# Performance work log

Measured on AMD Instinct MI355X. Metric: run time of the kernel, lower is better.

## Reference

```python
import jax, jax.numpy as jnp
import numpy as np

B, T, F, H, A, D = 1024, 256, 128, 128, 8, 256


def setup_inputs() -> dict:
    key = jax.random.key(0)
    ks = jax.random.split(key, 16)
    s = lambda k, shape, scale: jax.random.normal(k, shape, dtype=jnp.float32) * scale
    return {
        "h": jax.random.normal(ks[0], (B, T, F), dtype=jnp.float32),
        # LSTM params (flax LSTMCell: input kernel no bias, hidden kernel with bias; gate order i,f,g,o)
        "Wx": s(ks[1], (F, 4 * H), 1.0 / np.sqrt(F)),
        "Wh": s(ks[2], (H, 4 * H), 1.0 / np.sqrt(H)),
        "bh": jnp.zeros((4 * H,), jnp.float32),
        # actor head
        "Wa1": s(ks[3], (H, D), np.sqrt(2.0 / H)),
        "ba1": jnp.zeros((D,), jnp.float32),
        "Wa2": s(ks[4], (D, D), np.sqrt(2.0 / D)),
        "ba2": jnp.zeros((D,), jnp.float32),
        "Wa3": s(ks[5], (D, A), 0.01 / np.sqrt(D)),
        "ba3": jnp.zeros((A,), jnp.float32),
        "log_std": jnp.zeros((A,), jnp.float32),
        # critic head
        "Wc1": s(ks[6], (H, D), np.sqrt(2.0 / H)),
        "bc1": jnp.zeros((D,), jnp.float32),
        "Wc2": s(ks[7], (D, D), np.sqrt(2.0 / D)),
        "bc2": jnp.zeros((D,), jnp.float32),
        "Wc3": s(ks[8], (D, 1), 1.0 / np.sqrt(D)),
        "bc3": jnp.zeros((1,), jnp.float32),
    }


def reference(h, Wx, Wh, bh, Wa1, ba1, Wa2, ba2, Wa3, ba3, log_std,
              Wc1, bc1, Wc2, bc2, Wc3, bc3):
    act = jnp.tanh  # activation='tanh'
    # Precompute input projections for all gates: [B,T,4H] -> scan over time.
    xg = jnp.einsum('btf,fg->btg', h, Wx)
    c0 = jnp.zeros((h.shape[0], H), h.dtype)
    h0 = jnp.zeros((h.shape[0], H), h.dtype)

    def step(carry, xg_t):
        c, hs = carry
        z = xg_t + hs @ Wh + bh  # [B,4H]
        i = jax.nn.sigmoid(z[:, :H])
        f = jax.nn.sigmoid(z[:, H:2 * H])
        g = jnp.tanh(z[:, 2 * H:3 * H])
        o = jax.nn.sigmoid(z[:, 3 * H:])
        c = f * c + i * g
        hs = o * jnp.tanh(c)
        return (c, hs), None

    (_, x), _ = jax.lax.scan(step, (c0, h0), jnp.swapaxes(xg, 0, 1))  # x = last hidden [B,H]

    a = act(x @ Wa1 + ba1)
    a = act(a @ Wa2 + ba2)
    mean = a @ Wa3 + ba3                      # [B,A] policy mean
    std = jnp.exp(log_std)                    # [A] policy std (diag)

    v = act(x @ Wc1 + bc1)
    v = act(v @ Wc2 + bc2)
    value = (v @ Wc3 + bc3)                   # [B,1]

    # Pack (mean, std, value) as in (pi, critic): [B, 2A+1]
    return jnp.concatenate([mean, jnp.broadcast_to(std, mean.shape), value], axis=-1)
```

## Files before the change

### kernel.cpp

```cpp
#include <hip/hip_runtime.h>


typedef _Float16 f16x8 __attribute__((ext_vector_type(8)));
typedef _Float16 f16x4 __attribute__((ext_vector_type(4)));
typedef float    f32x4 __attribute__((ext_vector_type(4)));

#define NLOG2E (-1.4426950408889634f)

__device__ __forceinline__ float rcpf(float x) { return __builtin_amdgcn_rcpf(x); }
__device__ __forceinline__ float ex2(float x)  { return __builtin_amdgcn_exp2f(x); }

__device__ __forceinline__ f16x4 pack4(const float4 a) {
    f16x4 v;
    v[0] = (_Float16)a.x; v[1] = (_Float16)a.y;
    v[2] = (_Float16)a.z; v[3] = (_Float16)a.w;
    return v;
}

__global__ __launch_bounds__(512, 2)
void ac_fused(const float* __restrict__ hin,
              const float* __restrict__ Wx, const float* __restrict__ Wh,
              const float* __restrict__ bh,
              const float* __restrict__ Wa1, const float* __restrict__ ba1,
              const float* __restrict__ Wa2, const float* __restrict__ ba2,
              const float* __restrict__ Wa3, const float* __restrict__ ba3,
              const float* __restrict__ logstd,
              const float* __restrict__ Wc1, const float* __restrict__ bc1,
              const float* __restrict__ Wc2, const float* __restrict__ bc2,
              const float* __restrict__ Wc3, const float* __restrict__ bc3,
              float* __restrict__ out)
{
    constexpr int T = 256, F = 128, H = 128, G = 512;

    __shared__ f16x8 Abuf[2][256];
    __shared__ f16x8 Axg[2][256];
    __shared__ float xf[4][F + 1];
    __shared__ float hb[2][4][257];

    const int tid  = threadIdx.x;
    const int lane = tid & 63;
    const int wv   = tid >> 6;
    const int m16  = lane & 15;
    const int q    = lane >> 4;
    const int r0   = blockIdx.x << 2;
    const int ncol = (wv << 4) + m16;

    f16x8 bwx[4][4], bwh[4][4];
    #pragma unroll
    for (int kt = 0; kt < 4; ++kt) {
        #pragma unroll
        for (int s = 0; s < 4; ++s) {
            f16x8 vx, vh;
            #pragma unroll
            for (int j = 0; j < 8; ++j) {
                const int k = (kt << 5) + (q << 3) + j;
                vx[j] = (_Float16)Wx[k * G + s * H + ncol];
                vh[j] = (_Float16)Wh[k * G + s * H + ncol];
            }
            bwx[s][kt] = vx;
            bwh[s][kt] = vh;
        }
    }
    const float nbi = NLOG2E * bh[0 * H + ncol];
    const float nbf = NLOG2E * bh[1 * H + ncol];
    const float nbg = 2.0f * NLOG2E * bh[2 * H + ncol];
    const float nbo = NLOG2E * bh[3 * H + ncol];

    const int xc = tid >> 1;
    const int xh = tid & 1;
    const int xk0 = ((xc >> 6) << 5) + (((xc >> 4) & 3) << 3) + (xh << 2);
    const float* pgbase = hin + (size_t)(r0 + ((xc >> 2) & 3)) * T * F
                              + (size_t)(xc & 3) * F + xk0;

    const int hw0 = ((((ncol >> 5) << 6) + (((ncol >> 3) & 3) << 4) + (q << 2)) << 3)
                    + (ncol & 7);

    {
        f16x8 zz = {};
        ((f16x8*)Abuf)[tid] = zz;
    }

    {
        const float4 xp0 = *(const float4*)(pgbase);
        const float4 xp1 = *(const float4*)(pgbase + 4 * (size_t)F);
        __syncthreads();
        *(f16x4*)((_Float16*)&Axg[0][0] + xc * 8 + xh * 4) = pack4(xp0);
        *(f16x4*)((_Float16*)&Axg[1][0] + xc * 8 + xh * 4) = pack4(xp1);
    }
    asm volatile("s_waitcnt lgkmcnt(0)" ::: "memory");
    __builtin_amdgcn_s_barrier();

    float cstate = 0.0f;
    float hcur   = 0.0f;

    for (int t0 = 0; t0 < T; t0 += 8) {
        f32x4 P[2][4];
        #pragma unroll
        for (int mt = 0; mt < 2; ++mt)
            #pragma unroll
            for (int s = 0; s < 4; ++s) P[mt][s] = f32x4{0.f, 0.f, 0.f, 0.f};
        #pragma unroll
        for (int kt = 0; kt < 4; ++kt) {
            const f16x8 fr0 = Axg[0][(kt << 6) + lane];
            const f16x8 fr1 = Axg[1][(kt << 6) + lane];
            P[0][0] = __builtin_amdgcn_mfma_f32_16x16x32_f16(fr0, bwx[0][kt], P[0][0], 0, 0, 0);
            P[0][1] = __builtin_amdgcn_mfma_f32_16x16x32_f16(fr0, bwx[1][kt], P[0][1], 0, 0, 0);
            P[0][2] = __builtin_amdgcn_mfma_f32_16x16x32_f16(fr0, bwx[2][kt], P[0][2], 0, 0, 0);
            P[0][3] = __builtin_amdgcn_mfma_f32_16x16x32_f16(fr0, bwx[3][kt], P[0][3], 0, 0, 0);
            P[1][0] = __builtin_amdgcn_mfma_f32_16x16x32_f16(fr1, bwx[0][kt], P[1][0], 0, 0, 0);
            P[1][1] = __builtin_amdgcn_mfma_f32_16x16x32_f16(fr1, bwx[1][kt], P[1][1], 0, 0, 0);
            P[1][2] = __builtin_amdgcn_mfma_f32_16x16x32_f16(fr1, bwx[2][kt], P[1][2], 0, 0, 0);
            P[1][3] = __builtin_amdgcn_mfma_f32_16x16x32_f16(fr1, bwx[3][kt], P[1][3], 0, 0, 0);
        }

        float4 xp0n, xp1n;
        #pragma unroll
        for (int i = 0; i < 8; ++i) {
            const f16x8* Ac = &Abuf[i & 1][0];
            f16x8*       An = &Abuf[(i + 1) & 1][0];

            if (i == 2) {
                const int t0n = (t0 + 8 < T) ? t0 + 8 : t0;
                xp0n = *(const float4*)(pgbase + (size_t)t0n * F);
                xp1n = *(const float4*)(pgbase + (size_t)(t0n + 4) * F);
            }

            const f16x8 af0 = Ac[lane];
            const f16x8 af1 = Ac[64 + lane];
            const f16x8 af2 = Ac[128 + lane];
            const f16x8 af3 = Ac[192 + lane];

            const int mt = i >> 2, rg = i & 3;
            const float x0 = P[mt][0][rg], x1 = P[mt][1][rg];
            const float x2 = P[mt][2][rg], x3 = P[mt][3][rg];
            f32x4 a0 = {x0, x0, x0, x0}, a1 = {x1, x1, x1, x1};
            f32x4 a2 = {x2, x2, x2, x2}, a3 = {x3, x3, x3, x3};

            a0 = __builtin_amdgcn_mfma_f32_16x16x32_f16(af0, bwh[0][0], a0, 0, 0, 0);
            a1 = __builtin_amdgcn_mfma_f32_16x16x32_f16(af0, bwh[1][0], a1, 0, 0, 0);
            a2 = __builtin_amdgcn_mfma_f32_16x16x32_f16(af0, bwh[2][0], a2, 0, 0, 0);
            a3 = __builtin_amdgcn_mfma_f32_16x16x32_f16(af0, bwh[3][0], a3, 0, 0, 0);
            a0 = __builtin_amdgcn_mfma_f32_16x16x32_f16(af1, bwh[0][1], a0, 0, 0, 0);
            a1 = __builtin_amdgcn_mfma_f32_16x16x32_f16(af1, bwh[1][1], a1, 0, 0, 0);
            a2 = __builtin_amdgcn_mfma_f32_16x16x32_f16(af1, bwh[2][1], a2, 0, 0, 0);
            a3 = __builtin_amdgcn_mfma_f32_16x16x32_f16(af1, bwh[3][1], a3, 0, 0, 0);
            a0 = __builtin_amdgcn_mfma_f32_16x16x32_f16(af2, bwh[0][2], a0, 0, 0, 0);
            a1 = __builtin_amdgcn_mfma_f32_16x16x32_f16(af2, bwh[1][2], a1, 0, 0, 0);
            a2 = __builtin_amdgcn_mfma_f32_16x16x32_f16(af2, bwh[2][2], a2, 0, 0, 0);
            a3 = __builtin_amdgcn_mfma_f32_16x16x32_f16(af2, bwh[3][2], a3, 0, 0, 0);
            a0 = __builtin_amdgcn_mfma_f32_16x16x32_f16(af3, bwh[0][3], a0, 0, 0, 0);
            a1 = __builtin_amdgcn_mfma_f32_16x16x32_f16(af3, bwh[1][3], a1, 0, 0, 0);
            a2 = __builtin_amdgcn_mfma_f32_16x16x32_f16(af3, bwh[2][3], a2, 0, 0, 0);
            a3 = __builtin_amdgcn_mfma_f32_16x16x32_f16(af3, bwh[3][3], a3, 0, 0, 0);

            const float iv = rcpf(1.0f + ex2(fmaf(a0[0], NLOG2E, nbi)));
            const float fv = rcpf(1.0f + ex2(fmaf(a1[0], NLOG2E, nbf)));
            const float gv = 2.0f * rcpf(1.0f + ex2(fmaf(a2[0], 2.0f * NLOG2E, nbg))) - 1.0f;
            const float ov = rcpf(1.0f + ex2(fmaf(a3[0], NLOG2E, nbo)));
            cstate = fv * cstate + iv * gv;
            const float th = 2.0f * rcpf(1.0f + ex2(cstate * (2.0f * NLOG2E))) - 1.0f;
            hcur = ov * th;

            {
                const _Float16 hh = (_Float16)hcur;
                _Float16* hp = (_Float16*)An + hw0;
                hp[0]  = hh;
                hp[8]  = hh;
                hp[16] = hh;
                hp[24] = hh;
            }

            if (i == 7) {
                *(f16x4*)((_Float16*)&Axg[0][0] + xc * 8 + xh * 4) = pack4(xp0n);
                *(f16x4*)((_Float16*)&Axg[1][0] + xc * 8 + xh * 4) = pack4(xp1n);
            }

            asm volatile("s_waitcnt lgkmcnt(0)" ::: "memory");
            __builtin_amdgcn_s_barrier();
        }
    }

    xf[q][ncol] = hcur;
    __syncthreads();

    const int n  = tid & 255;
    const int rh = tid >> 8;

    auto tanhl = [&](float x) { return 2.0f * rcpf(1.0f + ex2(x * (2.0f * NLOG2E))) - 1.0f; };

    auto layer = [&](const float* __restrict__ W, const float* __restrict__ bv,
                     const float* xin, int xs, int K, float* yout, int ys) {
        float acc0, acc1;
        const float b = bv[n];
        acc0 = b; acc1 = b;
        #pragma unroll 4
        for (int k = 0; k < K; ++k) {
            const float w = W[k * 256 + n];
            acc0 += xin[(rh * 2 + 0) * xs + k] * w;
            acc1 += xin[(rh * 2 + 1) * xs + k] * w;
        }
        yout[(rh * 2 + 0) * ys + n] = tanhl(acc0);
        yout[(rh * 2 + 1) * ys + n] = tanhl(acc1);
    };

    layer(Wa1, ba1, &xf[0][0], F + 1, 128, &hb[0][0][0], 257);
    __syncthreads();
    layer(Wa2, ba2, &hb[0][0][0], 257, 256, &hb[1][0][0], 257);
    __syncthreads();
    layer(Wc1, bc1, &xf[0][0], F + 1, 128, &hb[0][0][0], 257);
    if (tid < 32) {
        const int r = tid >> 3, aa = tid & 7;
        float acc = ba3[aa];
        #pragma unroll 4
        for (int k = 0; k < 256; ++k) acc += hb[1][r][k] * Wa3[k * 8 + aa];
        out[(size_t)(r0 + r) * 17 + aa]     = acc;
        out[(size_t)(r0 + r) * 17 + 8 + aa] = __expf(logstd[aa]);
    }
    __syncthreads();
    layer(Wc2, bc2, &hb[0][0][0], 257, 256, &hb[1][0][0], 257);
    __syncthreads();
    if (tid < 4) {
        const int r = tid;
        float acc = bc3[0];
        #pragma unroll 4
        for (int k = 0; k < 256; ++k) acc += hb[1][r][k] * Wc3[k];
        out[(size_t)(r0 + r) * 17 + 16] = acc;
    }
}

extern "C" void kernel_launch(void* const* d_in, const int* in_sizes, int n_in,
                              void* d_out, int out_size, void* d_ws, size_t ws_size,
                              hipStream_t stream) {
    (void)in_sizes; (void)n_in; (void)d_ws; (void)ws_size; (void)out_size;
    const float* hin = (const float*)d_in[0];
    const float* Wx  = (const float*)d_in[1];
    const float* Wh  = (const float*)d_in[2];
    const float* bh  = (const float*)d_in[3];
    const float* Wa1 = (const float*)d_in[4];
    const float* ba1 = (const float*)d_in[5];
    const float* Wa2 = (const float*)d_in[6];
    const float* ba2 = (const float*)d_in[7];
    const float* Wa3 = (const float*)d_in[8];
    const float* ba3 = (const float*)d_in[9];
    const float* ls  = (const float*)d_in[10];
    const float* Wc1 = (const float*)d_in[11];
    const float* bc1 = (const float*)d_in[12];
    const float* Wc2 = (const float*)d_in[13];
    const float* bc2 = (const float*)d_in[14];
    const float* Wc3 = (const float*)d_in[15];
    const float* bc3 = (const float*)d_in[16];

    hipLaunchKernelGGL(ac_fused, dim3(256), dim3(512), 0, stream,
                       hin, Wx, Wh, bh, Wa1, ba1, Wa2, ba2, Wa3, ba3, ls,
                       Wc1, bc1, Wc2, bc2, Wc3, bc3, (float*)d_out);
}
```

Baseline: 425.6 us.

## Shrink hidden-state buffer, write h once, parallelize head reductions

The hidden-state LDS buffer is compacted from a replicated 256-entry A-fragment layout into a 16x4 layout. Each thread now writes its h value once instead of four times, and the MFMA A fragments are read with replicated row indices, which cuts LDS store traffic on the serial recurrent path. The final actor and critic projections are split across many threads with a partial-sum reduction in shared memory, in place of 32 or 4 threads running 256-long serial loops, and the MLP loop unroll factor is raised. The extra barriers and reduction buffers add a little overhead to the tail.

```diff
diff --git a/kernel.cpp b/kernel.cpp
--- a/kernel.cpp
+++ b/kernel.cpp
@@ -32,10 +32,12 @@
 {
     constexpr int T = 256, F = 128, H = 128, G = 512;
 
-    __shared__ f16x8 Abuf[2][256];
+    __shared__ f16x8 Hbuf[2][16][4];
     __shared__ f16x8 Axg[2][256];
     __shared__ float xf[4][F + 1];
     __shared__ float hb[2][4][257];
+    __shared__ float redA[4][8][8];
+    __shared__ float redC[4][32];
 
     const int tid  = threadIdx.x;
     const int lane = tid & 63;
@@ -72,12 +74,12 @@
     const float* pgbase = hin + (size_t)(r0 + ((xc >> 2) & 3)) * T * F
                               + (size_t)(xc & 3) * F + xk0;
 
-    const int hw0 = ((((ncol >> 5) << 6) + (((ncol >> 3) & 3) << 4) + (q << 2)) << 3)
-                    + (ncol & 7);
-
-    {
+    const int hr0 = (q << 2) + (m16 >> 2);
+    const int hw  = ((((ncol >> 3) << 2) + q) << 3) + (ncol & 7);
+
+    if (tid < 128) {
         f16x8 zz = {};
-        ((f16x8*)Abuf)[tid] = zz;
+        ((f16x8*)Hbuf)[tid] = zz;
     }
 
     {
@@ -116,8 +118,9 @@
         float4 xp0n, xp1n;
         #pragma unroll
         for (int i = 0; i < 8; ++i) {
-            const f16x8* Ac = &Abuf[i & 1][0];
-            f16x8*       An = &Abuf[(i + 1) & 1][0];
+            const int t = t0 + i;
+            const f16x8* Hc = &Hbuf[t & 1][0][0];
+            _Float16*    Hn = (_Float16*)&Hbuf[(t + 1) & 1][0][0];
 
             if (i == 2) {
                 const int t0n = (t0 + 8 < T) ? t0 + 8 : t0;
@@ -125,10 +128,10 @@
                 xp1n = *(const float4*)(pgbase + (size_t)(t0n + 4) * F);
             }
 
-            const f16x8 af0 = Ac[lane];
-            const f16x8 af1 = Ac[64 + lane];
-            const f16x8 af2 = Ac[128 + lane];
-            const f16x8 af3 = Ac[192 + lane];
+            const f16x8 af0 = Hc[hr0];
+            const f16x8 af1 = Hc[16 + hr0];
+            const f16x8 af2 = Hc[32 + hr0];
+            const f16x8 af3 = Hc[48 + hr0];
 
             const int mt = i >> 2, rg = i & 3;
             const float x0 = P[mt][0][rg], x1 = P[mt][1][rg];
@@ -161,14 +164,7 @@
             const float th = 2.0f * rcpf(1.0f + ex2(cstate * (2.0f * NLOG2E))) - 1.0f;
             hcur = ov * th;
 
-            {
-                const _Float16 hh = (_Float16)hcur;
-                _Float16* hp = (_Float16*)An + hw0;
-                hp[0]  = hh;
-                hp[8]  = hh;
-                hp[16] = hh;
-                hp[24] = hh;
-            }
+            Hn[hw] = (_Float16)hcur;
 
             if (i == 7) {
                 *(f16x4*)((_Float16*)&Axg[0][0] + xc * 8 + xh * 4) = pack4(xp0n);
@@ -193,7 +189,7 @@
         float acc0, acc1;
         const float b = bv[n];
         acc0 = b; acc1 = b;
-        #pragma unroll 4
+        #pragma unroll 16
         for (int k = 0; k < K; ++k) {
             const float w = W[k * 256 + n];
             acc0 += xin[(rh * 2 + 0) * xs + k] * w;
@@ -208,23 +204,39 @@
     layer(Wa2, ba2, &hb[0][0][0], 257, 256, &hb[1][0][0], 257);
     __syncthreads();
     layer(Wc1, bc1, &xf[0][0], F + 1, 128, &hb[0][0][0], 257);
+    if (tid < 256) {
+        const int r = tid >> 6, aa = (tid >> 3) & 7, seg = tid & 7;
+        float acc = 0.0f;
+        const int k0 = seg << 5;
+        #pragma unroll 16
+        for (int k = k0; k < k0 + 32; ++k) acc += hb[1][r][k] * Wa3[k * 8 + aa];
+        redA[r][aa][seg] = acc;
+    }
+    __syncthreads();
+    layer(Wc2, bc2, &hb[0][0][0], 257, 256, &hb[1][0][0], 257);
     if (tid < 32) {
         const int r = tid >> 3, aa = tid & 7;
         float acc = ba3[aa];
-        #pragma unroll 4
-        for (int k = 0; k < 256; ++k) acc += hb[1][r][k] * Wa3[k * 8 + aa];
+        #pragma unroll
+        for (int s = 0; s < 8; ++s) acc += redA[r][aa][s];
         out[(size_t)(r0 + r) * 17 + aa]     = acc;
         out[(size_t)(r0 + r) * 17 + 8 + aa] = __expf(logstd[aa]);
     }
     __syncthreads();
-    layer(Wc2, bc2, &hb[0][0][0], 257, 256, &hb[1][0][0], 257);
+    if (tid < 128) {
+        const int r = tid >> 5, seg = tid & 31;
+        float acc = 0.0f;
+        const int k0 = seg << 3;
+        #pragma unroll
+        for (int k = k0; k < k0 + 8; ++k) acc += hb[1][r][k] * Wc3[k];
+        redC[r][seg] = acc;
+    }
     __syncthreads();
     if (tid < 4) {
-        const int r = tid;
         float acc = bc3[0];
-        #pragma unroll 4
-        for (int k = 0; k < 256; ++k) acc += hb[1][r][k] * Wc3[k];
-        out[(size_t)(r0 + r) * 17 + 16] = acc;
+        #pragma unroll
+        for (int s = 0; s < 32; ++s) acc += redC[tid][s];
+        out[(size_t)(r0 + tid) * 17 + 16] = acc;
     }
 }
 
```

Result: faster. 348.9 us (-18.0%).
